# Kernel optimization log

Measured on AMD Instinct MI355X. Metric: run time of the kernel, lower is better.

The kernel has to match this reference:

```python
import jax, jax.numpy as jnp
import numpy as np

BATCH, DIN, DSTATE, DOUT = 16384, 1024, 2048, 1024


def setup_inputs() -> dict:
    key = jax.random.key(0)
    ks = jax.random.split(key, 8)
    return {
        "u_in": jax.random.normal(ks[0], (BATCH, 1, DIN), dtype=jnp.float32),
        "x_re": jnp.zeros((DSTATE,), dtype=jnp.float32),
        "x_im": jnp.zeros((DSTATE,), dtype=jnp.float32),
        "nu_log": jax.random.uniform(ks[1], (DSTATE,), dtype=jnp.float32),
        "theta_log": jax.random.uniform(ks[2], (DSTATE,), dtype=jnp.float32),
        "gamma_log": jax.random.uniform(ks[3], (DSTATE,), dtype=jnp.float32),
        "B_re": jax.random.normal(ks[4], (DSTATE, DIN), dtype=jnp.float32) / np.sqrt(2 * DIN).astype(np.float32),
        "B_im": jax.random.normal(ks[5], (DSTATE, DIN), dtype=jnp.float32) / np.sqrt(2 * DIN).astype(np.float32),
        "C_re": jax.random.normal(ks[6], (DOUT, DSTATE), dtype=jnp.float32) / np.sqrt(DSTATE).astype(np.float32),
        "C_im": jax.random.normal(ks[7], (DOUT, DSTATE), dtype=jnp.float32) / np.sqrt(DSTATE).astype(np.float32),
        "D": jax.random.normal(jax.random.fold_in(key, 99), (DOUT, DIN), dtype=jnp.float32) / np.sqrt(DIN).astype(np.float32),
    }


def reference(u_in, x_re, x_im, nu_log, theta_log, gamma_log, B_re, B_im, C_re, C_im, D):
    # Diagonal complex transition lambda = exp(-exp(nu_log)) * exp(i*exp(theta_log))
    lam_mod = jnp.exp(-jnp.exp(nu_log))            # [S]
    theta = jnp.exp(theta_log)                     # [S]
    lam_re = lam_mod * jnp.cos(theta)
    lam_im = lam_mod * jnp.sin(theta)
    gammas = jnp.exp(gamma_log)                    # [S]
    # Bu = B @ u (u is real, so complex matmul splits into two real GEMMs)
    Bu_re = jnp.einsum('boi,si->bos', u_in, B_re)  # [B,1,S]
    Bu_im = jnp.einsum('boi,si->bos', u_in, B_im)  # [B,1,S]
    # x_new = lambda * x + gamma * Bu   (complex, diagonal)
    xn_re = lam_re * x_re - lam_im * x_im + gammas * Bu_re
    xn_im = lam_re * x_im + lam_im * x_re + gammas * Bu_im
    # y = 2*Re(C @ x_new) + D @ u
    y = (2.0 * (jnp.einsum('bos,js->boj', xn_re, C_re)
                - jnp.einsum('bos,js->boj', xn_im, C_im))
         + jnp.einsum('boi,ji->boj', u_in, D))     # [B,1,O]
    return y
```

## Files before the change

kernel.cpp:

```cpp
#include <hip/hip_runtime.h>
#include <hip/hip_fp16.h>
#include <stdint.h>


typedef _Float16 f16x8 __attribute__((ext_vector_type(8)));
typedef __fp16 fp16x2 __attribute__((ext_vector_type(2)));
typedef float f32x4 __attribute__((ext_vector_type(4)));

#define GLOBAL_AS __attribute__((address_space(1)))
#define LDS_AS __attribute__((address_space(3)))

constexpr int BATCH = 16384, DIN = 1024, DSTATE = 2048, DOUT = 1024;
constexpr int S2 = 2 * DSTATE;
constexpr int KSPLIT = 4;

__device__ __forceinline__ int lds_off(int row, int k) {
  int slot = k >> 3;
  int sl = slot ^ ((row >> 1) & 3);
  return row * 64 + sl * 16 + (k & 7) * 2;
}

__global__ void k_state(const float* __restrict__ xr, const float* __restrict__ xi,
                        const float* __restrict__ nu, const float* __restrict__ th,
                        const float* __restrict__ ga, float* __restrict__ g,
                        float* __restrict__ cre, float* __restrict__ cim) {
  int s = blockIdx.x * 256 + threadIdx.x;
  if (s < DSTATE) {
    float lm = expf(-expf(nu[s]));
    float t = expf(th[s]);
    float lr = lm * cosf(t), li = lm * sinf(t);
    g[s] = expf(ga[s]);
    cre[s] = lr * xr[s] - li * xi[s];
    cim[s] = lr * xi[s] + li * xr[s];
  }
}

__global__ void k_y0(const float* __restrict__ cre, const float* __restrict__ cim,
                     const float* __restrict__ Cre, const float* __restrict__ Cim,
                     float* __restrict__ y0) {
  int j = blockIdx.x;
  float acc = 0.f;
  for (int s = threadIdx.x; s < DSTATE; s += 256)
    acc += cre[s] * Cre[(long)j * DSTATE + s] - cim[s] * Cim[(long)j * DSTATE + s];
  for (int off = 32; off; off >>= 1) acc += __shfl_down(acc, off);
  __shared__ float red[4];
  if ((threadIdx.x & 63) == 0) red[threadIdx.x >> 6] = acc;
  __syncthreads();
  if (threadIdx.x == 0) y0[j] = 2.f * (red[0] + red[1] + red[2] + red[3]);
}

__global__ void k_bgt(const float* __restrict__ Bre, const float* __restrict__ Bim,
                      const float* __restrict__ g, __half* __restrict__ Bh,
                      __half* __restrict__ Bl) {
  __shared__ float tile[32][33];
  int s0 = blockIdx.x * 32, i0 = blockIdx.y * 32;
  int c = threadIdx.x & 31, r0 = threadIdx.x >> 5;
  const float* src = (s0 < DSTATE) ? Bre : Bim;
  int sbase = (s0 < DSTATE) ? s0 : s0 - DSTATE;
  for (int rr = 0; rr < 32; rr += 8) {
    int s = sbase + r0 + rr;
    tile[r0 + rr][c] = src[(long)s * DIN + i0 + c] * (256.f * g[s]);
  }
  __syncthreads();
  for (int rr = 0; rr < 32; rr += 8) {
    int i = i0 + r0 + rr;
    float v = tile[c][r0 + rr];
    __half h = __float2half(v);
    __half l = __float2half(v - __half2float(h));
    Bh[(long)i * S2 + s0 + c] = h;
    Bl[(long)i * S2 + s0 + c] = l;
  }
}

template <int BM, int BN, int EPI, int ASRC>
__global__ __launch_bounds__(256, 2) void k_gemm(
    const float* __restrict__ A, const float* __restrict__ A2,
    const __half* __restrict__ Bh, const __half* __restrict__ Bl,
    const float* __restrict__ extra, float* __restrict__ outF,
    int M, int N, int K, int kiters) {
  constexpr int FM = BM / 32;
  constexpr int FN = BN / 32;
  constexpr int ASPL = (EPI == 0) ? 2 : 1;
  constexpr int ABYTES = BM * 64;
  constexpr int BBYTES = BN * 64;
  __shared__ alignas(16) char smem[ASPL * ABYTES + 2 * BBYTES];
  char* sAh = smem;
  char* sAl = smem + ABYTES;
  char* sBh = smem + ASPL * ABYTES;
  char* sBl = smem + ASPL * ABYTES + BBYTES;

  const int tid = threadIdx.x;
  const int lane = tid & 63;
  const int wid = tid >> 6;
  const int wr = wid >> 1, wc = wid & 1;
  int bm0, bn0, kb;
  if constexpr (EPI == 1) {
    int wg = blockIdx.x;
    int lin = (wg & 7) * 128 + (wg >> 3);
    bm0 = (lin >> 3) * BM;
    bn0 = (lin & 7) * BN;
    kb = 0;
  } else {
    bm0 = blockIdx.y * BM;
    bn0 = blockIdx.x * BN;
    kb = blockIdx.z * (S2 / KSPLIT);
  }
  const int r16 = lane & 15;
  const int ksl = lane >> 4;

  f32x4 acc[FM][FN];
#pragma unroll
  for (int i = 0; i < FM; ++i)
#pragma unroll
    for (int j = 0; j < FN; ++j) acc[i][j] = f32x4{0.f, 0.f, 0.f, 0.f};

  constexpr int APT = (BM * 8) / 256;
  constexpr int IPW = (BN / 16) / 4;

  for (int kt = 0; kt < kiters; ++kt) {
    __syncthreads();
#pragma unroll
    for (int it = 0; it < APT; ++it) {
      int idx = it * 256 + tid;
      int row = idx >> 3;
      int k0 = (idx & 7) * 4;
      f32x4 v;
      if (ASRC == 0) {
        v = *(const f32x4*)(A + (long)(bm0 + row) * K + kb + kt * 32 + k0);
      } else {
        int s = kb + kt * 32 + k0;
        const float* src = (s < DSTATE) ? A : A2;
        int sc = (s < DSTATE) ? s : s - DSTATE;
        v = *(const f32x4*)(src + (long)(bm0 + row) * DSTATE + sc);
        v *= (s < DSTATE) ? 512.f : -512.f;
      }
      int off = lds_off(row, k0);
      if constexpr (EPI == 1) {
        union { uint32_t w[2]; uint64_t u; } p;
        fp16x2 h0 = __builtin_amdgcn_cvt_pkrtz(v[0], v[1]);
        fp16x2 h1 = __builtin_amdgcn_cvt_pkrtz(v[2], v[3]);
        p.w[0] = __builtin_bit_cast(uint32_t, h0);
        p.w[1] = __builtin_bit_cast(uint32_t, h1);
        *(uint64_t*)(sAh + off) = p.u;
      } else {
        union { __half h[4]; uint64_t u; } ph, pl;
#pragma unroll
        for (int j = 0; j < 4; ++j) {
          __half hh = __float2half(v[j]);
          ph.h[j] = hh;
          pl.h[j] = __float2half(v[j] - __half2float(hh));
        }
        *(uint64_t*)(sAh + off) = ph.u;
        *(uint64_t*)(sAl + off) = pl.u;
      }
    }
#pragma unroll
    for (int ii = 0; ii < IPW; ++ii) {
      int inst = wid * IPW + ii;
      int row = inst * 16 + (lane >> 2);
      int slot = (lane & 3) ^ ((row >> 1) & 3);
      const __half* gh = Bh + (long)(bn0 + row) * K + kb + kt * 32 + slot * 8;
      const __half* gl = Bl + (long)(bn0 + row) * K + kb + kt * 32 + slot * 8;
      __builtin_amdgcn_global_load_lds((GLOBAL_AS const unsigned int*)gh,
                                       (LDS_AS unsigned int*)(sBh + inst * 1024), 16, 0, 0);
      __builtin_amdgcn_global_load_lds((GLOBAL_AS const unsigned int*)gl,
                                       (LDS_AS unsigned int*)(sBl + inst * 1024), 16, 0, 0);
    }
    __syncthreads();
    f16x8 ah[FM], bh[FN], bl[FN];
    f16x8 al[FM];
#pragma unroll
    for (int m = 0; m < FM; ++m) {
      int row = wr * (BM / 2) + m * 16 + r16;
      ah[m] = *(const f16x8*)(sAh + lds_off(row, ksl * 8));
      if constexpr (EPI == 0) al[m] = *(const f16x8*)(sAl + lds_off(row, ksl * 8));
    }
#pragma unroll
    for (int n = 0; n < FN; ++n) {
      int row = wc * (BN / 2) + n * 16 + r16;
      bh[n] = *(const f16x8*)(sBh + lds_off(row, ksl * 8));
      bl[n] = *(const f16x8*)(sBl + lds_off(row, ksl * 8));
    }
#pragma unroll
    for (int m = 0; m < FM; ++m)
#pragma unroll
      for (int n = 0; n < FN; ++n)
        acc[m][n] = __builtin_amdgcn_mfma_f32_16x16x32_f16(ah[m], bh[n], acc[m][n], 0, 0, 0);
#pragma unroll
    for (int m = 0; m < FM; ++m)
#pragma unroll
      for (int n = 0; n < FN; ++n)
        acc[m][n] = __builtin_amdgcn_mfma_f32_16x16x32_f16(ah[m], bl[n], acc[m][n], 0, 0, 0);
    if constexpr (EPI == 0) {
#pragma unroll
      for (int m = 0; m < FM; ++m)
#pragma unroll
        for (int n = 0; n < FN; ++n)
          acc[m][n] = __builtin_amdgcn_mfma_f32_16x16x32_f16(al[m], bh[n], acc[m][n], 0, 0, 0);
    }
  }

  const int rowb = (lane >> 4) * 4;
#pragma unroll
  for (int m = 0; m < FM; ++m)
#pragma unroll
    for (int n = 0; n < FN; ++n)
#pragma unroll
      for (int r = 0; r < 4; ++r) {
        int gr = bm0 + wr * (BM / 2) + m * 16 + rowb + r;
        int gc = bn0 + wc * (BN / 2) + n * 16 + r16;
        if constexpr (EPI == 0) {
          outF[(long)blockIdx.z * M * N + (long)gr * N + gc] = acc[m][n][r];
        } else {
          outF[(long)gr * N + gc] = acc[m][n][r] * (1.f / 256.f) + extra[gc];
        }
      }
}

__global__ void k_redM(const float* __restrict__ P, const float* __restrict__ D,
                       __half* __restrict__ Mh, __half* __restrict__ Ml) {
  int idx = (blockIdx.x * 256 + threadIdx.x) * 4;
  f32x4 s = *(const f32x4*)(P + idx);
  s += *(const f32x4*)(P + (1 << 20) + idx);
  s += *(const f32x4*)(P + (2 << 20) + idx);
  s += *(const f32x4*)(P + (3 << 20) + idx);
  f32x4 d = *(const f32x4*)(D + idx);
  union { __half h[4]; uint64_t u; } ph, pl;
#pragma unroll
  for (int j = 0; j < 4; ++j) {
    float v = s[j] * (1.f / 256.f) + 256.f * d[j];
    __half hh = __float2half(v);
    ph.h[j] = hh;
    pl.h[j] = __float2half(v - __half2float(hh));
  }
  *(uint64_t*)(Mh + idx) = ph.u;
  *(uint64_t*)(Ml + idx) = pl.u;
}

extern "C" void kernel_launch(void* const* d_in, const int* in_sizes, int n_in,
                              void* d_out, int out_size, void* d_ws, size_t ws_size,
                              hipStream_t stream) {
  const float* u   = (const float*)d_in[0];
  const float* xr  = (const float*)d_in[1];
  const float* xi  = (const float*)d_in[2];
  const float* nu  = (const float*)d_in[3];
  const float* th  = (const float*)d_in[4];
  const float* ga  = (const float*)d_in[5];
  const float* Bre = (const float*)d_in[6];
  const float* Bim = (const float*)d_in[7];
  const float* Cre = (const float*)d_in[8];
  const float* Cim = (const float*)d_in[9];
  const float* Dm  = (const float*)d_in[10];
  float* y = (float*)d_out;

  char* w = (char*)d_ws;
  float* g   = (float*)(w);
  float* cre = (float*)(w + 8192);
  float* cim = (float*)(w + 16384);
  float* y0  = (float*)(w + 24576);
  __half* Bgh = (__half*)(w + 32768);
  __half* Bgl = (__half*)(w + 32768 + 8388608);
  __half* Mh  = (__half*)(w + 32768 + 2 * 8388608);
  __half* Ml  = (__half*)(w + 32768 + 2 * 8388608 + 2097152);
  float* Mpart = (float*)(w + 32768 + 2 * 8388608 + 2 * 2097152);

  k_state<<<DSTATE / 256, 256, 0, stream>>>(xr, xi, nu, th, ga, g, cre, cim);
  k_y0<<<DOUT, 256, 0, stream>>>(cre, cim, Cre, Cim, y0);
  k_bgt<<<dim3(S2 / 32, DIN / 32), 256, 0, stream>>>(Bre, Bim, g, Bgh, Bgl);
  k_gemm<64, 64, 0, 1><<<dim3(DIN / 64, DOUT / 64, KSPLIT), 256, 0, stream>>>(
      Cre, Cim, Bgh, Bgl, nullptr, Mpart, DOUT, DIN, S2, (S2 / KSPLIT) / 32);
  k_redM<<<1024, 256, 0, stream>>>(Mpart, Dm, Mh, Ml);
  k_gemm<128, 128, 1, 0><<<(BATCH / 128) * (DOUT / 128), 256, 0, stream>>>(
      u, nullptr, Mh, Ml, y0, y, BATCH, DOUT, DIN, DIN / 32);
}
```

Baseline: 280.5 us.

## Fuse state kernel, atomic split-K for M, drop A-split, retile precompute GEMM

Removes k_state by computing expf(ga) inside k_bgt and recomputing lambda and the state inside k_y0. The precompute GEMM M = C·B·gamma now uses 128x128 tiles with KSPLIT=8 and accumulates with atomicAdd into a zeroed buffer, so the reduction kernel reads one partial instead of four. The A operand is now converted to a single fp16 value with round-to-nearest in both GEMMs, which drops the low-part MFMA pass in the first GEMM but lowers precision for C. The main batch GEMM now uses round-to-nearest instead of round-toward-zero conversion, and the extra memset plus atomics add some cost.

```diff
diff --git a/kernel.cpp b/kernel.cpp
--- a/kernel.cpp
+++ b/kernel.cpp
@@ -4,7 +4,6 @@
 
 
 typedef _Float16 f16x8 __attribute__((ext_vector_type(8)));
-typedef __fp16 fp16x2 __attribute__((ext_vector_type(2)));
 typedef float f32x4 __attribute__((ext_vector_type(4)));
 
 #define GLOBAL_AS __attribute__((address_space(1)))
@@ -12,7 +11,7 @@
 
 constexpr int BATCH = 16384, DIN = 1024, DSTATE = 2048, DOUT = 1024;
 constexpr int S2 = 2 * DSTATE;
-constexpr int KSPLIT = 4;
+constexpr int KSPLIT = 8;
 
 __device__ __forceinline__ int lds_off(int row, int k) {
   int slot = k >> 3;
@@ -20,37 +19,8 @@
   return row * 64 + sl * 16 + (k & 7) * 2;
 }
 
-__global__ void k_state(const float* __restrict__ xr, const float* __restrict__ xi,
-                        const float* __restrict__ nu, const float* __restrict__ th,
-                        const float* __restrict__ ga, float* __restrict__ g,
-                        float* __restrict__ cre, float* __restrict__ cim) {
-  int s = blockIdx.x * 256 + threadIdx.x;
-  if (s < DSTATE) {
-    float lm = expf(-expf(nu[s]));
-    float t = expf(th[s]);
-    float lr = lm * cosf(t), li = lm * sinf(t);
-    g[s] = expf(ga[s]);
-    cre[s] = lr * xr[s] - li * xi[s];
-    cim[s] = lr * xi[s] + li * xr[s];
-  }
-}
-
-__global__ void k_y0(const float* __restrict__ cre, const float* __restrict__ cim,
-                     const float* __restrict__ Cre, const float* __restrict__ Cim,
-                     float* __restrict__ y0) {
-  int j = blockIdx.x;
-  float acc = 0.f;
-  for (int s = threadIdx.x; s < DSTATE; s += 256)
-    acc += cre[s] * Cre[(long)j * DSTATE + s] - cim[s] * Cim[(long)j * DSTATE + s];
-  for (int off = 32; off; off >>= 1) acc += __shfl_down(acc, off);
-  __shared__ float red[4];
-  if ((threadIdx.x & 63) == 0) red[threadIdx.x >> 6] = acc;
-  __syncthreads();
-  if (threadIdx.x == 0) y0[j] = 2.f * (red[0] + red[1] + red[2] + red[3]);
-}
-
 __global__ void k_bgt(const float* __restrict__ Bre, const float* __restrict__ Bim,
-                      const float* __restrict__ g, __half* __restrict__ Bh,
+                      const float* __restrict__ ga, __half* __restrict__ Bh,
                       __half* __restrict__ Bl) {
   __shared__ float tile[32][33];
   int s0 = blockIdx.x * 32, i0 = blockIdx.y * 32;
@@ -59,7 +29,7 @@
   int sbase = (s0 < DSTATE) ? s0 : s0 - DSTATE;
   for (int rr = 0; rr < 32; rr += 8) {
     int s = sbase + r0 + rr;
-    tile[r0 + rr][c] = src[(long)s * DIN + i0 + c] * (256.f * g[s]);
+    tile[r0 + rr][c] = src[(long)s * DIN + i0 + c] * (256.f * expf(ga[s]));
   }
   __syncthreads();
   for (int rr = 0; rr < 32; rr += 8) {
@@ -72,7 +42,28 @@
   }
 }
 
-template <int BM, int BN, int EPI, int ASRC>
+__global__ void k_y0(const float* __restrict__ xr, const float* __restrict__ xi,
+                     const float* __restrict__ nu, const float* __restrict__ th,
+                     const float* __restrict__ Cre, const float* __restrict__ Cim,
+                     float* __restrict__ y0) {
+  int j = blockIdx.x;
+  float acc = 0.f;
+  for (int s = threadIdx.x; s < DSTATE; s += 256) {
+    float lm = expf(-expf(nu[s]));
+    float t = expf(th[s]);
+    float lr = lm * cosf(t), li = lm * sinf(t);
+    float cr = lr * xr[s] - li * xi[s];
+    float ci = lr * xi[s] + li * xr[s];
+    acc += cr * Cre[(long)j * DSTATE + s] - ci * Cim[(long)j * DSTATE + s];
+  }
+  for (int off = 32; off; off >>= 1) acc += __shfl_down(acc, off);
+  __shared__ float red[4];
+  if ((threadIdx.x & 63) == 0) red[threadIdx.x >> 6] = acc;
+  __syncthreads();
+  if (threadIdx.x == 0) y0[j] = 2.f * (red[0] + red[1] + red[2] + red[3]);
+}
+
+template <int BM, int BN, int AMODE, int EPI>
 __global__ __launch_bounds__(256, 2) void k_gemm(
     const float* __restrict__ A, const float* __restrict__ A2,
     const __half* __restrict__ Bh, const __half* __restrict__ Bl,
@@ -80,14 +71,12 @@
     int M, int N, int K, int kiters) {
   constexpr int FM = BM / 32;
   constexpr int FN = BN / 32;
-  constexpr int ASPL = (EPI == 0) ? 2 : 1;
   constexpr int ABYTES = BM * 64;
   constexpr int BBYTES = BN * 64;
-  __shared__ alignas(16) char smem[ASPL * ABYTES + 2 * BBYTES];
-  char* sAh = smem;
-  char* sAl = smem + ABYTES;
-  char* sBh = smem + ASPL * ABYTES;
-  char* sBl = smem + ASPL * ABYTES + BBYTES;
+  __shared__ alignas(16) char smem[ABYTES + 2 * BBYTES];
+  char* sA = smem;
+  char* sBh = smem + ABYTES;
+  char* sBl = smem + ABYTES + BBYTES;
 
   const int tid = threadIdx.x;
   const int lane = tid & 63;
@@ -125,7 +114,7 @@
       int row = idx >> 3;
       int k0 = (idx & 7) * 4;
       f32x4 v;
-      if (ASRC == 0) {
+      if constexpr (AMODE == 2) {
         v = *(const f32x4*)(A + (long)(bm0 + row) * K + kb + kt * 32 + k0);
       } else {
         int s = kb + kt * 32 + k0;
@@ -134,25 +123,10 @@
         v = *(const f32x4*)(src + (long)(bm0 + row) * DSTATE + sc);
         v *= (s < DSTATE) ? 512.f : -512.f;
       }
-      int off = lds_off(row, k0);
-      if constexpr (EPI == 1) {
-        union { uint32_t w[2]; uint64_t u; } p;
-        fp16x2 h0 = __builtin_amdgcn_cvt_pkrtz(v[0], v[1]);
-        fp16x2 h1 = __builtin_amdgcn_cvt_pkrtz(v[2], v[3]);
-        p.w[0] = __builtin_bit_cast(uint32_t, h0);
-        p.w[1] = __builtin_bit_cast(uint32_t, h1);
-        *(uint64_t*)(sAh + off) = p.u;
-      } else {
-        union { __half h[4]; uint64_t u; } ph, pl;
-#pragma unroll
-        for (int j = 0; j < 4; ++j) {
-          __half hh = __float2half(v[j]);
-          ph.h[j] = hh;
-          pl.h[j] = __float2half(v[j] - __half2float(hh));
-        }
-        *(uint64_t*)(sAh + off) = ph.u;
-        *(uint64_t*)(sAl + off) = pl.u;
-      }
+      union { __half h[4]; uint64_t u; } p;
+#pragma unroll
+      for (int j = 0; j < 4; ++j) p.h[j] = __float2half(v[j]);
+      *(uint64_t*)(sA + lds_off(row, k0)) = p.u;
     }
 #pragma unroll
     for (int ii = 0; ii < IPW; ++ii) {
@@ -167,13 +141,11 @@
                                        (LDS_AS unsigned int*)(sBl + inst * 1024), 16, 0, 0);
     }
     __syncthreads();
-    f16x8 ah[FM], bh[FN], bl[FN];
-    f16x8 al[FM];
+    f16x8 a[FM], bh[FN], bl[FN];
 #pragma unroll
     for (int m = 0; m < FM; ++m) {
       int row = wr * (BM / 2) + m * 16 + r16;
-      ah[m] = *(const f16x8*)(sAh + lds_off(row, ksl * 8));
-      if constexpr (EPI == 0) al[m] = *(const f16x8*)(sAl + lds_off(row, ksl * 8));
+      a[m] = *(const f16x8*)(sA + lds_off(row, ksl * 8));
     }
 #pragma unroll
     for (int n = 0; n < FN; ++n) {
@@ -185,19 +157,12 @@
     for (int m = 0; m < FM; ++m)
 #pragma unroll
       for (int n = 0; n < FN; ++n)
-        acc[m][n] = __builtin_amdgcn_mfma_f32_16x16x32_f16(ah[m], bh[n], acc[m][n], 0, 0, 0);
+        acc[m][n] = __builtin_amdgcn_mfma_f32_16x16x32_f16(a[m], bh[n], acc[m][n], 0, 0, 0);
 #pragma unroll
     for (int m = 0; m < FM; ++m)
 #pragma unroll
       for (int n = 0; n < FN; ++n)
-        acc[m][n] = __builtin_amdgcn_mfma_f32_16x16x32_f16(ah[m], bl[n], acc[m][n], 0, 0, 0);
-    if constexpr (EPI == 0) {
-#pragma unroll
-      for (int m = 0; m < FM; ++m)
-#pragma unroll
-        for (int n = 0; n < FN; ++n)
-          acc[m][n] = __builtin_amdgcn_mfma_f32_16x16x32_f16(al[m], bh[n], acc[m][n], 0, 0, 0);
-    }
+        acc[m][n] = __builtin_amdgcn_mfma_f32_16x16x32_f16(a[m], bl[n], acc[m][n], 0, 0, 0);
   }
 
   const int rowb = (lane >> 4) * 4;
@@ -210,7 +175,7 @@
         int gr = bm0 + wr * (BM / 2) + m * 16 + rowb + r;
         int gc = bn0 + wc * (BN / 2) + n * 16 + r16;
         if constexpr (EPI == 0) {
-          outF[(long)blockIdx.z * M * N + (long)gr * N + gc] = acc[m][n][r];
+          atomicAdd(outF + (long)gr * N + gc, acc[m][n][r]);
         } else {
           outF[(long)gr * N + gc] = acc[m][n][r] * (1.f / 256.f) + extra[gc];
         }
@@ -221,9 +186,6 @@
                        __half* __restrict__ Mh, __half* __restrict__ Ml) {
   int idx = (blockIdx.x * 256 + threadIdx.x) * 4;
   f32x4 s = *(const f32x4*)(P + idx);
-  s += *(const f32x4*)(P + (1 << 20) + idx);
-  s += *(const f32x4*)(P + (2 << 20) + idx);
-  s += *(const f32x4*)(P + (3 << 20) + idx);
   f32x4 d = *(const f32x4*)(D + idx);
   union { __half h[4]; uint64_t u; } ph, pl;
 #pragma unroll
@@ -254,22 +216,19 @@
   float* y = (float*)d_out;
 
   char* w = (char*)d_ws;
-  float* g   = (float*)(w);
-  float* cre = (float*)(w + 8192);
-  float* cim = (float*)(w + 16384);
-  float* y0  = (float*)(w + 24576);
-  __half* Bgh = (__half*)(w + 32768);
-  __half* Bgl = (__half*)(w + 32768 + 8388608);
-  __half* Mh  = (__half*)(w + 32768 + 2 * 8388608);
-  __half* Ml  = (__half*)(w + 32768 + 2 * 8388608 + 2097152);
-  float* Mpart = (float*)(w + 32768 + 2 * 8388608 + 2 * 2097152);
-
-  k_state<<<DSTATE / 256, 256, 0, stream>>>(xr, xi, nu, th, ga, g, cre, cim);
-  k_y0<<<DOUT, 256, 0, stream>>>(cre, cim, Cre, Cim, y0);
-  k_bgt<<<dim3(S2 / 32, DIN / 32), 256, 0, stream>>>(Bre, Bim, g, Bgh, Bgl);
-  k_gemm<64, 64, 0, 1><<<dim3(DIN / 64, DOUT / 64, KSPLIT), 256, 0, stream>>>(
+  float* y0  = (float*)(w);
+  __half* Bgh = (__half*)(w + 65536);
+  __half* Bgl = (__half*)(w + 65536 + 8388608);
+  __half* Mh  = (__half*)(w + 65536 + 16777216);
+  __half* Ml  = (__half*)(w + 65536 + 16777216 + 2097152);
+  float* Mpart = (float*)(w + 65536 + 16777216 + 4194304);
+
+  hipMemsetAsync(Mpart, 0, (size_t)DOUT * DIN * 4, stream);
+  k_bgt<<<dim3(S2 / 32, DIN / 32), 256, 0, stream>>>(Bre, Bim, ga, Bgh, Bgl);
+  k_y0<<<DOUT, 256, 0, stream>>>(xr, xi, nu, th, Cre, Cim, y0);
+  k_gemm<128, 128, 1, 0><<<dim3(DIN / 128, DOUT / 128, KSPLIT), 256, 0, stream>>>(
       Cre, Cim, Bgh, Bgl, nullptr, Mpart, DOUT, DIN, S2, (S2 / KSPLIT) / 32);
   k_redM<<<1024, 256, 0, stream>>>(Mpart, Dm, Mh, Ml);
-  k_gemm<128, 128, 1, 0><<<(BATCH / 128) * (DOUT / 128), 256, 0, stream>>>(
+  k_gemm<128, 128, 2, 1><<<(BATCH / 128) * (DOUT / 128), 256, 0, stream>>>(
       u, nullptr, Mh, Ml, y0, y, BATCH, DOUT, DIN, DIN / 32);
 }
```

After: 290.4 us. +3.5%, slower.
